# Performance work log

Hardware: AMD Instinct MI355X
Metric: run time of the kernel (lower is better)

## Reference

```python
import jax, jax.numpy as jnp
import numpy as np

V = 100000
E = 1250000
C_IN = 64
C_OUT = 64


def setup_inputs() -> dict:
    key = jax.random.key(0)
    ks = jax.random.split(key, 6)
    X = jax.random.normal(ks[0], (V, C_IN), dtype=jnp.float32)
    edge_src = jax.random.randint(ks[1], (E,), 0, V, dtype=jnp.int32)
    edge_dst = jax.random.randint(ks[2], (E,), 0, V, dtype=jnp.int32)
    edge_w = jax.random.uniform(ks[3], (E,), dtype=jnp.float32)
    # xavier_normal for (C_IN, C_OUT) weight
    std = float(np.sqrt(2.0 / (C_IN + C_OUT)))
    W = jax.random.normal(ks[4], (C_IN, C_OUT), dtype=jnp.float32) * std
    b = jax.random.normal(ks[5], (C_OUT,), dtype=jnp.float32) * 0.0  # bias init zeros
    return {"X": X, "edge_src": edge_src, "edge_dst": edge_dst,
            "edge_w": edge_w, "W": W, "b": b}


def reference(X, edge_src, edge_dst, edge_w, W, b):
    # f = A @ X  (sparse COO spmm): f[dst] += w * X[src]
    msgs = edge_w[:, None] * X[edge_src]                 # [E, C_IN]
    f = jax.ops.segment_sum(msgs, edge_dst, num_segments=X.shape[0])  # [V, C_IN]
    # out = f @ W + b
    return f @ W + b
```

## Files before the change

kernel.cpp:

```cpp
#include <hip/hip_runtime.h>
#include <hip/hip_fp16.h>


constexpr int V = 100000;
constexpr int E = 1250000;
constexpr int C = 64;

constexpr int NBKT = 1024;
constexpr int VB   = 98;
constexpr int BCAP = 1536;
constexpr int FL   = 8;
constexpr int OVF_CAP = 16384;

constexpr size_t Y_OFF    = 0;
constexpr size_t BIN_OFF  = 12800000;
constexpr size_t GCNT_OFF = 25382912;
constexpr size_t OC_OFF   = 25387008;
constexpr size_t OVF_OFF  = 25387024;
constexpr size_t WS_NEW   = 25649168;

using bf16x8 = __attribute__((ext_vector_type(8))) short;
using f32x4  = __attribute__((ext_vector_type(4))) float;

__device__ __forceinline__ short f2bf(float x) {
    unsigned u = __float_as_uint(x);
    unsigned r = u + 0x7fffu + ((u >> 16) & 1u);
    return (short)(r >> 16);
}
__device__ __forceinline__ float bf2f(short h) {
    return __uint_as_float(((unsigned)(unsigned short)h) << 16);
}

__global__ __launch_bounds__(256) void zero_kernel(int* __restrict__ gcnt,
                                                   int* __restrict__ oc) {
    int i = threadIdx.x;
    #pragma unroll
    for (int j = 0; j < NBKT / 256; ++j) gcnt[i + j * 256] = 0;
    if (i == 0) *oc = 0;
}

constexpr int FUSE_T    = 512;
constexpr int XWB       = 782;
constexpr int BINB      = 512;
constexpr int FUSE_GRID = 261 * 5;

__global__ __launch_bounds__(FUSE_T) void xwbin_kernel(
        const float* __restrict__ X,
        const float* __restrict__ W,
        __half*      __restrict__ Y,
        const int*   __restrict__ esrc,
        const int*   __restrict__ edst,
        const float* __restrict__ ew,
        int*  __restrict__ gcnt,
        int2* __restrict__ binned,
        int*  __restrict__ oc,
        int4* __restrict__ ovf) {
    __shared__ union {
        struct { short Whi[64 * 72]; short Wlo[64 * 72]; } xw;
        struct { int2 stage[NBKT][FL]; int lcnt[NBKT]; } bin;
    } u;

    const int grp  = blockIdx.x / 5;
    const int slot = blockIdx.x % 5;

    if (slot < 3) {
        const int xb = grp * 3 + slot;
        if (xb >= XWB) return;

        for (int idx = threadIdx.x; idx < 4096; idx += FUSE_T) {
            int k = idx >> 6, c = idx & 63;
            float w  = W[idx];
            short hi = f2bf(w);
            short lo = f2bf(w - bf2f(hi));
            u.xw.Whi[c * 72 + k] = hi;
            u.xw.Wlo[c * 72 + k] = lo;
        }
        __syncthreads();

        const int wave = threadIdx.x >> 6;
        const int lane = threadIdx.x & 63;
        const int m = lane & 15;
        const int q = lane >> 4;

        bf16x8 bhi[4][2], blo[4][2];
        #pragma unroll
        for (int t = 0; t < 4; ++t)
            #pragma unroll
            for (int h = 0; h < 2; ++h) {
                int o = (t * 16 + m) * 72 + h * 32 + q * 8;
                bhi[t][h] = *(const bf16x8*)&u.xw.Whi[o];
                blo[t][h] = *(const bf16x8*)&u.xw.Wlo[o];
            }

        const int chunk = xb * 8 + wave;
        if (chunk >= V / 16) return;
        {
            const float* xp = X + (chunk * 16 + m) * 64 + q * 8;
            bf16x8 ahi[2], alo[2];
            #pragma unroll
            for (int h = 0; h < 2; ++h) {
                float4 f0 = *(const float4*)(xp + h * 32);
                float4 f1 = *(const float4*)(xp + h * 32 + 4);
                float f[8] = {f0.x, f0.y, f0.z, f0.w, f1.x, f1.y, f1.z, f1.w};
                #pragma unroll
                for (int j = 0; j < 8; ++j) {
                    short hi = f2bf(f[j]);
                    ahi[h][j] = hi;
                    alo[h][j] = f2bf(f[j] - bf2f(hi));
                }
            }
            #pragma unroll
            for (int t = 0; t < 4; ++t) {
                f32x4 acc = {0.f, 0.f, 0.f, 0.f};
                #pragma unroll
                for (int h = 0; h < 2; ++h) {
                    acc = __builtin_amdgcn_mfma_f32_16x16x32_bf16(ahi[h], bhi[t][h], acc, 0, 0, 0);
                    acc = __builtin_amdgcn_mfma_f32_16x16x32_bf16(alo[h], bhi[t][h], acc, 0, 0, 0);
                    acc = __builtin_amdgcn_mfma_f32_16x16x32_bf16(ahi[h], blo[t][h], acc, 0, 0, 0);
                }
                #pragma unroll
                for (int i = 0; i < 4; ++i) {
                    int row = chunk * 16 + q * 4 + i;
                    Y[row * 64 + t * 16 + m] = __float2half(acc[i]);
                }
            }
        }
    } else {
        const int bb = grp * 2 + (slot - 3);
        if (bb >= BINB) return;

        for (int i = threadIdx.x; i < NBKT; i += FUSE_T) u.bin.lcnt[i] = 0;
        __syncthreads();

        const int iters = (E + BINB * FUSE_T - 1) / (BINB * FUSE_T);
        for (int it = 0; it < iters; ++it) {
            int e = (it * BINB + bb) * FUSE_T + threadIdx.x;
            if (e < E) {
                int d = edst[e];
                int s = esrc[e];
                float w = ew[e];
                int bkt = d / VB;
                int ld  = d - bkt * VB;
                int2 rec = make_int2((ld << 17) | s, __float_as_int(w));
                int pos = atomicAdd(&u.bin.lcnt[bkt], 1);
                if (pos < FL) {
                    u.bin.stage[bkt][pos] = rec;
                } else {
                    int g = atomicAdd(&gcnt[bkt], 1);
                    if (g < BCAP) binned[bkt * BCAP + g] = rec;
                    else { int p = atomicAdd(oc, 1);
                           if (p < OVF_CAP) ovf[p] = make_int4(s, d, __float_as_int(w), 0); }
                }
            }
        }
        __syncthreads();
        for (int b = threadIdx.x; b < NBKT; b += FUSE_T) {
            int n = u.bin.lcnt[b]; n = n < FL ? n : FL;
            if (n > 0) {
                int g = atomicAdd(&gcnt[b], n);
                for (int i = 0; i < n; ++i) {
                    int gi = g + i;
                    int2 r = u.bin.stage[b][i];
                    if (gi < BCAP) binned[b * BCAP + gi] = r;
                    else { int s = r.x & 0x1FFFF; int ld = r.x >> 17;
                           int p = atomicAdd(oc, 1);
                           if (p < OVF_CAP) ovf[p] = make_int4(s, b * VB + ld, r.y, 0); }
                }
            }
        }
    }
}

__global__ __launch_bounds__(512) void bucket_gather_kernel(const int*  __restrict__ gcnt,
                                                            const int2* __restrict__ binned,
                                                            const int*  __restrict__ oc,
                                                            const int4* __restrict__ ovf,
                                                            const __half* __restrict__ Y,
                                                            const float* __restrict__ bias,
                                                            float* __restrict__ out) {
    __shared__ int2 raw[BCAP];
    __shared__ int2 sorted[BCAP];
    __shared__ int  cnt[VB];
    __shared__ int  pre[VB];
    __shared__ int  cur[VB];
    __shared__ int  buf[128];

    const int tid = threadIdx.x;
    const int b   = blockIdx.x;
    int n = gcnt[b]; n = n < BCAP ? n : BCAP;

    for (int i = tid; i < VB; i += 512) cnt[i] = 0;
    __syncthreads();

    const int2* src = binned + b * BCAP;
    for (int i = tid; i < n; i += 512) {
        int2 r = src[i];
        raw[i] = r;
        atomicAdd(&cnt[r.x >> 17], 1);
    }
    __syncthreads();

    int x = 0;
    if (tid < 128) { x = (tid < VB) ? cnt[tid] : 0; buf[tid] = x; }
    __syncthreads();
    #pragma unroll
    for (int ofs = 1; ofs < 128; ofs <<= 1) {
        int t = 0;
        if (tid < 128 && tid >= ofs) t = buf[tid - ofs];
        __syncthreads();
        if (tid < 128) buf[tid] += t;
        __syncthreads();
    }
    if (tid < VB) { int ex = buf[tid] - x; pre[tid] = ex; cur[tid] = ex; }
    __syncthreads();

    for (int i = tid; i < n; i += 512) {
        int2 r = raw[i];
        int ld = r.x >> 17;
        int p = atomicAdd(&cur[ld], 1);
        sorted[p] = r;
    }
    __syncthreads();

    const int lane = tid & 63;
    const int wv   = tid >> 6;
    float bias_l = bias[lane];
    int ovn = *oc; ovn = ovn < OVF_CAP ? ovn : OVF_CAP;

    for (int ld = wv; ld < VB; ld += 8) {
        int v = b * VB + ld;
        if (v >= V) break;
        int beg = pre[ld];
        int end = beg + cnt[ld];
        float acc = 0.f;
        int i = beg;
        for (; i + 8 <= end; i += 8) {
            int2 r0 = sorted[i],     r1 = sorted[i + 1];
            int2 r2 = sorted[i + 2], r3 = sorted[i + 3];
            int2 r4 = sorted[i + 4], r5 = sorted[i + 5];
            int2 r6 = sorted[i + 6], r7 = sorted[i + 7];
            float y0 = __half2float(Y[(r0.x & 0x1FFFF) * C + lane]);
            float y1 = __half2float(Y[(r1.x & 0x1FFFF) * C + lane]);
            float y2 = __half2float(Y[(r2.x & 0x1FFFF) * C + lane]);
            float y3 = __half2float(Y[(r3.x & 0x1FFFF) * C + lane]);
            float y4 = __half2float(Y[(r4.x & 0x1FFFF) * C + lane]);
            float y5 = __half2float(Y[(r5.x & 0x1FFFF) * C + lane]);
            float y6 = __half2float(Y[(r6.x & 0x1FFFF) * C + lane]);
            float y7 = __half2float(Y[(r7.x & 0x1FFFF) * C + lane]);
            acc += __int_as_float(r0.y) * y0;
            acc += __int_as_float(r1.y) * y1;
            acc += __int_as_float(r2.y) * y2;
            acc += __int_as_float(r3.y) * y3;
            acc += __int_as_float(r4.y) * y4;
            acc += __int_as_float(r5.y) * y5;
            acc += __int_as_float(r6.y) * y6;
            acc += __int_as_float(r7.y) * y7;
        }
        for (; i + 4 <= end; i += 4) {
            int2 r0 = sorted[i], r1 = sorted[i + 1], r2 = sorted[i + 2], r3 = sorted[i + 3];
            float y0 = __half2float(Y[(r0.x & 0x1FFFF) * C + lane]);
            float y1 = __half2float(Y[(r1.x & 0x1FFFF) * C + lane]);
            float y2 = __half2float(Y[(r2.x & 0x1FFFF) * C + lane]);
            float y3 = __half2float(Y[(r3.x & 0x1FFFF) * C + lane]);
            acc += __int_as_float(r0.y) * y0;
            acc += __int_as_float(r1.y) * y1;
            acc += __int_as_float(r2.y) * y2;
            acc += __int_as_float(r3.y) * y3;
        }
        for (; i < end; ++i) {
            int2 rr = sorted[i];
            acc += __int_as_float(rr.y) * __half2float(Y[(rr.x & 0x1FFFF) * C + lane]);
        }
        for (int k = 0; k < ovn; ++k) {
            int4 rr = ovf[k];
            if (rr.y == v)
                acc += __int_as_float(rr.z) * __half2float(Y[rr.x * C + lane]);
        }
        out[v * C + lane] = acc + bias_l;
    }
}

__global__ __launch_bounds__(256) void xw_kernel(const float* __restrict__ X,
                                                 const float* __restrict__ W,
                                                 float* __restrict__ Y) {
    __shared__ float Ws[64][64];
    const float4* W4 = (const float4*)W;
    float4* Ws4 = (float4*)&Ws[0][0];
    #pragma unroll
    for (int i = 0; i < 4; ++i)
        Ws4[threadIdx.x + 256 * i] = W4[threadIdx.x + 256 * i];
    __syncthreads();
    const int wave = threadIdx.x >> 6;
    const int lane = threadIdx.x & 63;
    for (int row = blockIdx.x * 4 + wave; row < V; row += gridDim.x * 4) {
        float xv = X[row * C + lane];
        float acc = 0.f;
        #pragma unroll
        for (int k = 0; k < C; ++k)
            acc += __shfl(xv, k, 64) * Ws[k][lane];
        Y[row * C + lane] = acc;
    }
}

__global__ __launch_bounds__(256) void init_out_kernel(const float* __restrict__ b,
                                                       float4* __restrict__ out4) {
    int tid = blockIdx.x * 256 + threadIdx.x;
    const int n4 = V * (C / 4);
    if (tid < n4) {
        const float4* b4 = (const float4*)b;
        out4[tid] = b4[tid & 15];
    }
}

__global__ __launch_bounds__(256) void scatter_kernel(const int*   __restrict__ esrc,
                                                      const int*   __restrict__ edst,
                                                      const float* __restrict__ ew,
                                                      const float* __restrict__ Y,
                                                      float*       __restrict__ out) {
    unsigned tid = blockIdx.x * 256u + threadIdx.x;
    unsigned e = tid >> 4;
    if (e >= (unsigned)E) return;
    int g = (tid & 15) * 4;
    int   s  = esrc[e];
    int   d  = edst[e];
    float we = ew[e];
    float4 y = *(const float4*)(Y + s * C + g);
    float* o = out + (size_t)d * C + g;
    atomicAdd(o + 0, we * y.x);
    atomicAdd(o + 1, we * y.y);
    atomicAdd(o + 2, we * y.z);
    atomicAdd(o + 3, we * y.w);
}

extern "C" void kernel_launch(void* const* d_in, const int* in_sizes, int n_in,
                              void* d_out, int out_size, void* d_ws, size_t ws_size,
                              hipStream_t stream) {
    const float* X    = (const float*)d_in[0];
    const int*   esrc = (const int*)  d_in[1];
    const int*   edst = (const int*)  d_in[2];
    const float* ew   = (const float*)d_in[3];
    const float* W    = (const float*)d_in[4];
    const float* b    = (const float*)d_in[5];
    float* out = (float*)d_out;

    char* ws = (char*)d_ws;

    if (ws_size >= WS_NEW) {
        __half* Y     = (__half*)(ws + Y_OFF);
        int2*  binned = (int2*)(ws + BIN_OFF);
        int*   gcnt   = (int*) (ws + GCNT_OFF);
        int*   oc     = (int*) (ws + OC_OFF);
        int4*  ovf    = (int4*)(ws + OVF_OFF);

        zero_kernel<<<1, 256, 0, stream>>>(gcnt, oc);
        xwbin_kernel<<<FUSE_GRID, FUSE_T, 0, stream>>>(X, W, Y, esrc, edst, ew,
                                                       gcnt, binned, oc, ovf);
        bucket_gather_kernel<<<NBKT, 512, 0, stream>>>(gcnt, binned, oc, ovf, Y, b, out);
    } else {
        float* Y = (float*)(ws + Y_OFF);
        xw_kernel<<<1024, 256, 0, stream>>>(X, W, Y);
        init_out_kernel<<<(V * (C / 4) + 255) / 256, 256, 0, stream>>>(b, (float4*)out);
        scatter_kernel<<<(E * 16 + 255) / 256, 256, 0, stream>>>(esrc, edst, ew, Y, out);
    }
}
```

Baseline: 140.0 us.

## Replace per-bucket counting sort with LDS atomic accumulation in gather

The gather kernel no longer counting-sorts each bucket's edges by local destination (histogram, prefix scan, scatter). Instead every wave walks the unsorted edge list and atomically adds weighted Y rows into a per-block LDS accumulator of VB×64 floats. The overflow list is also split across waves rather than scanned in full by every destination. This removes several barriers and a sort pass. The cost is LDS float atomics, which can contend on high-degree destinations, and about 25KB of extra shared memory per block that may lower occupancy.

Result: slower. 534.6 us (+281.8%).

```diff
diff --git a/kernel.cpp b/kernel.cpp
--- a/kernel.cpp
+++ b/kernel.cpp
@@ -178,105 +178,66 @@
                                                             const __half* __restrict__ Y,
                                                             const float* __restrict__ bias,
                                                             float* __restrict__ out) {
-    __shared__ int2 raw[BCAP];
-    __shared__ int2 sorted[BCAP];
-    __shared__ int  cnt[VB];
-    __shared__ int  pre[VB];
-    __shared__ int  cur[VB];
-    __shared__ int  buf[128];
+    __shared__ int2  raw[BCAP];
+    __shared__ float acc[VB * 64];
 
     const int tid = threadIdx.x;
     const int b   = blockIdx.x;
     int n = gcnt[b]; n = n < BCAP ? n : BCAP;
 
-    for (int i = tid; i < VB; i += 512) cnt[i] = 0;
-    __syncthreads();
-
+    for (int i = tid; i < VB * 64; i += 512) acc[i] = 0.f;
     const int2* src = binned + b * BCAP;
-    for (int i = tid; i < n; i += 512) {
-        int2 r = src[i];
-        raw[i] = r;
-        atomicAdd(&cnt[r.x >> 17], 1);
-    }
-    __syncthreads();
-
-    int x = 0;
-    if (tid < 128) { x = (tid < VB) ? cnt[tid] : 0; buf[tid] = x; }
-    __syncthreads();
-    #pragma unroll
-    for (int ofs = 1; ofs < 128; ofs <<= 1) {
-        int t = 0;
-        if (tid < 128 && tid >= ofs) t = buf[tid - ofs];
-        __syncthreads();
-        if (tid < 128) buf[tid] += t;
-        __syncthreads();
-    }
-    if (tid < VB) { int ex = buf[tid] - x; pre[tid] = ex; cur[tid] = ex; }
-    __syncthreads();
-
-    for (int i = tid; i < n; i += 512) {
-        int2 r = raw[i];
-        int ld = r.x >> 17;
-        int p = atomicAdd(&cur[ld], 1);
-        sorted[p] = r;
-    }
+    for (int i = tid; i < n; i += 512) raw[i] = src[i];
     __syncthreads();
 
     const int lane = tid & 63;
     const int wv   = tid >> 6;
+
+    int i = wv;
+    for (; i + 56 < n; i += 64) {
+        int2 r0 = raw[i],      r1 = raw[i + 8];
+        int2 r2 = raw[i + 16], r3 = raw[i + 24];
+        int2 r4 = raw[i + 32], r5 = raw[i + 40];
+        int2 r6 = raw[i + 48], r7 = raw[i + 56];
+        float y0 = __half2float(Y[(r0.x & 0x1FFFF) * C + lane]);
+        float y1 = __half2float(Y[(r1.x & 0x1FFFF) * C + lane]);
+        float y2 = __half2float(Y[(r2.x & 0x1FFFF) * C + lane]);
+        float y3 = __half2float(Y[(r3.x & 0x1FFFF) * C + lane]);
+        float y4 = __half2float(Y[(r4.x & 0x1FFFF) * C + lane]);
+        float y5 = __half2float(Y[(r5.x & 0x1FFFF) * C + lane]);
+        float y6 = __half2float(Y[(r6.x & 0x1FFFF) * C + lane]);
+        float y7 = __half2float(Y[(r7.x & 0x1FFFF) * C + lane]);
+        atomicAdd(&acc[(r0.x >> 17) * 64 + lane], __int_as_float(r0.y) * y0);
+        atomicAdd(&acc[(r1.x >> 17) * 64 + lane], __int_as_float(r1.y) * y1);
+        atomicAdd(&acc[(r2.x >> 17) * 64 + lane], __int_as_float(r2.y) * y2);
+        atomicAdd(&acc[(r3.x >> 17) * 64 + lane], __int_as_float(r3.y) * y3);
+        atomicAdd(&acc[(r4.x >> 17) * 64 + lane], __int_as_float(r4.y) * y4);
+        atomicAdd(&acc[(r5.x >> 17) * 64 + lane], __int_as_float(r5.y) * y5);
+        atomicAdd(&acc[(r6.x >> 17) * 64 + lane], __int_as_float(r6.y) * y6);
+        atomicAdd(&acc[(r7.x >> 17) * 64 + lane], __int_as_float(r7.y) * y7);
+    }
+    for (; i < n; i += 8) {
+        int2 r = raw[i];
+        float y = __half2float(Y[(r.x & 0x1FFFF) * C + lane]);
+        atomicAdd(&acc[(r.x >> 17) * 64 + lane], __int_as_float(r.y) * y);
+    }
+
+    int ovn = *oc; ovn = ovn < OVF_CAP ? ovn : OVF_CAP;
+    for (int k = wv; k < ovn; k += 8) {
+        int4 rr = ovf[k];
+        int d = rr.y;
+        if (d / VB == b) {
+            float y = __half2float(Y[rr.x * C + lane]);
+            atomicAdd(&acc[(d - b * VB) * 64 + lane], __int_as_float(rr.z) * y);
+        }
+    }
+    __syncthreads();
+
     float bias_l = bias[lane];
-    int ovn = *oc; ovn = ovn < OVF_CAP ? ovn : OVF_CAP;
-
     for (int ld = wv; ld < VB; ld += 8) {
         int v = b * VB + ld;
         if (v >= V) break;
-        int beg = pre[ld];
-        int end = beg + cnt[ld];
-        float acc = 0.f;
-        int i = beg;
-        for (; i + 8 <= end; i += 8) {
-            int2 r0 = sorted[i],     r1 = sorted[i + 1];
-            int2 r2 = sorted[i + 2], r3 = sorted[i + 3];
-            int2 r4 = sorted[i + 4], r5 = sorted[i + 5];
-            int2 r6 = sorted[i + 6], r7 = sorted[i + 7];
-            float y0 = __half2float(Y[(r0.x & 0x1FFFF) * C + lane]);
-            float y1 = __half2float(Y[(r1.x & 0x1FFFF) * C + lane]);
-            float y2 = __half2float(Y[(r2.x & 0x1FFFF) * C + lane]);
-            float y3 = __half2float(Y[(r3.x & 0x1FFFF) * C + lane]);
-            float y4 = __half2float(Y[(r4.x & 0x1FFFF) * C + lane]);
-            float y5 = __half2float(Y[(r5.x & 0x1FFFF) * C + lane]);
-            float y6 = __half2float(Y[(r6.x & 0x1FFFF) * C + lane]);
-            float y7 = __half2float(Y[(r7.x & 0x1FFFF) * C + lane]);
-            acc += __int_as_float(r0.y) * y0;
-            acc += __int_as_float(r1.y) * y1;
-            acc += __int_as_float(r2.y) * y2;
-            acc += __int_as_float(r3.y) * y3;
-            acc += __int_as_float(r4.y) * y4;
-            acc += __int_as_float(r5.y) * y5;
-            acc += __int_as_float(r6.y) * y6;
-            acc += __int_as_float(r7.y) * y7;
-        }
-        for (; i + 4 <= end; i += 4) {
-            int2 r0 = sorted[i], r1 = sorted[i + 1], r2 = sorted[i + 2], r3 = sorted[i + 3];
-            float y0 = __half2float(Y[(r0.x & 0x1FFFF) * C + lane]);
-            float y1 = __half2float(Y[(r1.x & 0x1FFFF) * C + lane]);
-            float y2 = __half2float(Y[(r2.x & 0x1FFFF) * C + lane]);
-            float y3 = __half2float(Y[(r3.x & 0x1FFFF) * C + lane]);
-            acc += __int_as_float(r0.y) * y0;
-            acc += __int_as_float(r1.y) * y1;
-            acc += __int_as_float(r2.y) * y2;
-            acc += __int_as_float(r3.y) * y3;
-        }
-        for (; i < end; ++i) {
-            int2 rr = sorted[i];
-            acc += __int_as_float(rr.y) * __half2float(Y[(rr.x & 0x1FFFF) * C + lane]);
-        }
-        for (int k = 0; k < ovn; ++k) {
-            int4 rr = ovf[k];
-            if (rr.y == v)
-                acc += __int_as_float(rr.z) * __half2float(Y[rr.x * C + lane]);
-        }
-        out[v * C + lane] = acc + bias_l;
+        out[v * C + lane] = acc[ld * 64 + lane] + bias_l;
     }
 }
 
```
